# Kernel optimization log

Measured on AMD Instinct MI355X. Metric: run time of the kernel, lower is better.

## Reference

```python
import jax, jax.numpy as jnp
import numpy as np

N_NODES = 100000
N_EDGES = 3200000
D_IN = 128
D_OUT = 128


def setup_inputs() -> dict:
    key = jax.random.key(0)
    k1, k2, k3, k4, k5 = jax.random.split(key, 5)
    input_feature = jax.random.normal(k1, (N_NODES, D_IN), dtype=jnp.float32)
    edge_src = jax.random.randint(k2, (N_EDGES,), 0, N_NODES, dtype=jnp.int32)
    edge_dst = jax.random.randint(k3, (N_EDGES,), 0, N_NODES, dtype=jnp.int32)
    edge_vals = jax.random.uniform(k4, (N_EDGES,), dtype=jnp.float32)
    # kaiming-uniform-like init for weight, zeros for bias (as in reset_parameters)
    bound = float(np.sqrt(6.0 / D_IN))
    weight = jax.random.uniform(k5, (D_IN, D_OUT), dtype=jnp.float32,
                                minval=-bound, maxval=bound)
    bias = jnp.zeros((D_OUT,), dtype=jnp.float32)
    return {
        "input_feature": input_feature,
        "edge_src": edge_src,
        "edge_dst": edge_dst,
        "edge_vals": edge_vals,
        "weight": weight,
        "bias": bias,
    }


def reference(input_feature, edge_src, edge_dst, edge_vals, weight, bias):
    # support = X @ W  -> [N, D_OUT]
    support = jnp.matmul(input_feature, weight)
    # sparse.mm(A, support): out[dst] += A[dst, src] * support[src]
    gathered = support[edge_src] * edge_vals[:, None]  # [E, D_OUT]
    output = jax.ops.segment_sum(gathered, edge_dst, num_segments=N_NODES)
    output = output + bias  # bias-add (use_bias=True)
    return output
```

## Files before the change

### kernel.cpp

```cpp
#include <hip/hip_runtime.h>

#define N_NODES 100000
#define N_EDGES 3200000
#define D 128

#define K1C    391
#define CHUNK  4096
#define NCHUNK 782
#define GEMMB  782
#define CAPB   8960

static const size_t OFF_SB    = 0;
static const size_t OFF_REC   = 25600000;
static const size_t OFF_SORT2 = 53626880;
static const size_t OFF_OFFS  = 67640320;
static const size_t OFF_GCUR  = 68040320;

typedef __attribute__((ext_vector_type(8))) short bf16x8;
typedef __attribute__((ext_vector_type(4))) float f32x4;

__device__ __forceinline__ unsigned short f2bf(float f) {
    unsigned u = __float_as_uint(f);
    return (unsigned short)((u + 0x7FFFu + ((u >> 16) & 1u)) >> 16);
}

__global__ __launch_bounds__(512) void partition_edges(
        const int* __restrict__ esrc,
        const int* __restrict__ edst,
        const float* __restrict__ eval,
        int* __restrict__ gcursor,
        int2* __restrict__ rec_out) {
    __shared__ int  hist[K1C];
    __shared__ int  lofs[K1C];
    __shared__ int  gbase[K1C];
    __shared__ int  cur[K1C];
    __shared__ int  wsum[8];
    __shared__ int2 staged[CHUNK];
    __shared__ unsigned short bkt[CHUNK];

    const int t    = threadIdx.x;
    const int lane = t & 63;
    const int wave = t >> 6;
    const int e0   = blockIdx.x * CHUNK;
    const int cnt  = min(CHUNK, N_EDGES - e0);

    for (int i = t; i < K1C; i += 512) hist[i] = 0;
    __syncthreads();

    for (int i = t; i < cnt; i += 512)
        atomicAdd(&hist[edst[e0 + i] >> 8], 1);
    __syncthreads();

    int hv   = (t < K1C) ? hist[t] : 0;
    int incl = hv;
    for (int off = 1; off < 64; off <<= 1) {
        int u = __shfl_up(incl, off);
        if (lane >= off) incl += u;
    }
    if (lane == 63) wsum[wave] = incl;
    __syncthreads();
    {
        int pre = 0;
        for (int w = 0; w < wave; ++w) pre += wsum[w];
        if (t < K1C) {
            int excl = pre + incl - hv;
            lofs[t]  = excl;
            cur[t]   = excl;
            gbase[t] = hv ? (t * CAPB + atomicAdd(&gcursor[t], hv)) : 0;
        }
    }
    __syncthreads();

    for (int i = t; i < cnt; i += 512) {
        int e = e0 + i;
        int d = edst[e];
        int b = d >> 8;
        int pos = atomicAdd(&cur[b], 1);
        staged[pos] = make_int2(esrc[e] | ((d & 255) << 17), __float_as_int(eval[e]));
        bkt[pos] = (unsigned short)b;
    }
    __syncthreads();

    for (int i = t; i < cnt; i += 512) {
        int bb = bkt[i];
        rec_out[gbase[bb] + (i - lofs[bb])] = staged[i];
    }
}

__global__ __launch_bounds__(256) void gemm_and_fine(
        const float* __restrict__ X,
        const float* __restrict__ W,
        unsigned* __restrict__ Sb,
        const int2* __restrict__ rec,
        const int* __restrict__ gcnt,
        int* __restrict__ offs,
        unsigned* __restrict__ sorted1) {
    __shared__ __align__(16) union {
        unsigned short wfrag[8][4][64][8];
        unsigned       stage[4][32][68];
    } u;
    __shared__ int fh[256];
    __shared__ int fcur[256];
    __shared__ int fwsum[4];

    const int t    = threadIdx.x;
    const int lane = t & 63;
    const int wave = t >> 6;

    if (blockIdx.x < GEMMB) {
        const int quad = lane >> 4;
        const int li   = lane & 15;
        const int rowBase = blockIdx.x * 128;

        for (int i = t; i < D * D; i += 256) {
            int k = i >> 7, n = i & 127;
            u.wfrag[n >> 4][k >> 5][((k >> 3) & 3) * 16 + (n & 15)][k & 7] = f2bf(W[i]);
        }
        __syncthreads();

        f32x4 acc[2][8];
#pragma unroll
        for (int rt = 0; rt < 2; ++rt)
#pragma unroll
            for (int ct = 0; ct < 8; ++ct)
                acc[rt][ct] = (f32x4){0.f, 0.f, 0.f, 0.f};

#pragma unroll
        for (int kt = 0; kt < 4; ++kt) {
            bf16x8 a[2];
#pragma unroll
            for (int rt = 0; rt < 2; ++rt) {
                int row = rowBase + wave * 32 + rt * 16 + li;
                if (row >= N_NODES) row = N_NODES - 1;
                const float* xp = X + (size_t)row * D + kt * 32 + quad * 8;
                float4 f0 = ((const float4*)xp)[0];
                float4 f1 = ((const float4*)xp)[1];
                bf16x8 av;
                av[0] = (short)f2bf(f0.x); av[1] = (short)f2bf(f0.y);
                av[2] = (short)f2bf(f0.z); av[3] = (short)f2bf(f0.w);
                av[4] = (short)f2bf(f1.x); av[5] = (short)f2bf(f1.y);
                av[6] = (short)f2bf(f1.z); av[7] = (short)f2bf(f1.w);
                a[rt] = av;
            }
#pragma unroll
            for (int ct = 0; ct < 8; ++ct) {
                bf16x8 b = *(const bf16x8*)&u.wfrag[ct][kt][lane][0];
                acc[0][ct] = __builtin_amdgcn_mfma_f32_16x16x32_bf16(a[0], b, acc[0][ct], 0, 0, 0);
                acc[1][ct] = __builtin_amdgcn_mfma_f32_16x16x32_bf16(a[1], b, acc[1][ct], 0, 0, 0);
            }
        }
        __syncthreads();

        unsigned short* sw = (unsigned short*)&u.stage[wave][0][0];
#pragma unroll
        for (int rt = 0; rt < 2; ++rt)
#pragma unroll
            for (int r = 0; r < 4; ++r) {
                int lrow = rt * 16 + quad * 4 + r;
#pragma unroll
                for (int ct = 0; ct < 8; ++ct)
                    sw[lrow * 136 + ct * 16 + li] = f2bf(acc[rt][ct][r]);
            }
        for (int lrow = 0; lrow < 32; ++lrow) {
            int node = rowBase + wave * 32 + lrow;
            if (node < N_NODES)
                Sb[(size_t)node * 64 + lane] = ((unsigned*)sw)[lrow * 68 + lane];
        }
    } else {
        const int c    = blockIdx.x - GEMMB;
        const int beg  = c * CAPB;
        const int bcnt = gcnt[c];
        const int end  = beg + bcnt;

        fh[t] = 0;
        __syncthreads();

        for (int i = beg + t; i < end; i += 256)
            atomicAdd(&fh[(rec[i].x >> 17) & 255], 1);
        __syncthreads();

        int hv   = fh[t];
        int incl = hv;
        for (int off = 1; off < 64; off <<= 1) {
            int uu = __shfl_up(incl, off);
            if (lane >= off) incl += uu;
        }
        if (lane == 63) fwsum[wave] = incl;
        __syncthreads();
        {
            int pre = 0;
            for (int w = 0; w < wave; ++w) pre += fwsum[w];
            int excl = pre + incl - hv;
            int node = c * 256 + t;
            if (node < N_NODES) offs[node] = beg + excl;
            fcur[t] = beg + excl;
        }
        __syncthreads();

        for (int i = beg + t; i < end; i += 256) {
            int2 q = rec[i];
            int dl = (q.x >> 17) & 255;
            int p = atomicAdd(&fcur[dl], 1);
            unsigned vb = f2bf(__int_as_float(q.y));
            sorted1[p] = (unsigned)(q.x & 0x1FFFF) | ((vb & 0x7FFFu) << 17);
        }
    }
}

#define FMA8(v, p) {                                                         \
    a0 += (v) * __uint_as_float((p).x << 16);                                \
    a1 += (v) * __uint_as_float((p).x & 0xFFFF0000u);                        \
    a2 += (v) * __uint_as_float((p).y << 16);                                \
    a3 += (v) * __uint_as_float((p).y & 0xFFFF0000u);                        \
    a4 += (v) * __uint_as_float((p).z << 16);                                \
    a5 += (v) * __uint_as_float((p).z & 0xFFFF0000u);                        \
    a6 += (v) * __uint_as_float((p).w << 16);                                \
    a7 += (v) * __uint_as_float((p).w & 0xFFFF0000u);                        \
}

__global__ __launch_bounds__(256) void reduce_segments(
        const unsigned* __restrict__ Sb,
        const unsigned* __restrict__ sorted,
        const int* __restrict__ offs,
        const int* __restrict__ gcnt,
        const float* __restrict__ bias,
        float* __restrict__ out) {
    const int lane = threadIdx.x & 63;
    const int node = (blockIdx.x * 256 + threadIdx.x) >> 6;
    if (node >= N_NODES) return;

    const int qr = lane >> 4;
    const int ql = lane & 15;

    const int beg = offs[node];
    const bool blast = ((node & 255) == 255) || (node == N_NODES - 1);
    const int end = blast ? ((node >> 8) * CAPB + gcnt[node >> 8])
                          : offs[node + 1];

    float a0 = 0.f, a1 = 0.f, a2 = 0.f, a3 = 0.f;
    float a4 = 0.f, a5 = 0.f, a6 = 0.f, a7 = 0.f;

    for (int base = beg; base < end; base += 64) {
        const int m = min(64, end - base);
        unsigned rec = 0;
        if (base + lane < end) rec = sorted[base + lane];
        const int ng = (m + 3) >> 2;

        int g = 0;
        for (; g + 4 <= ng; g += 4) {
            int i0 = 4 * (g + 0) + qr, i1 = 4 * (g + 1) + qr;
            int i2 = 4 * (g + 2) + qr, i3 = 4 * (g + 3) + qr;
            unsigned r0 = (unsigned)__shfl((int)rec, i0);
            unsigned r1 = (unsigned)__shfl((int)rec, i1);
            unsigned r2 = (unsigned)__shfl((int)rec, i2);
            unsigned r3 = (unsigned)__shfl((int)rec, i3);
            int s0 = r0 & 0x1FFFF, s1 = r1 & 0x1FFFF;
            int s2 = r2 & 0x1FFFF, s3 = r3 & 0x1FFFF;
            float v0 = __uint_as_float((r0 >> 17) << 16);
            float v1 = __uint_as_float((r1 >> 17) << 16);
            float v2 = __uint_as_float((r2 >> 17) << 16);
            float v3 = __uint_as_float((r3 >> 17) << 16);
            uint4 p0 = ((const uint4*)(Sb + (size_t)s0 * 64))[ql];
            uint4 p1 = ((const uint4*)(Sb + (size_t)s1 * 64))[ql];
            uint4 p2 = ((const uint4*)(Sb + (size_t)s2 * 64))[ql];
            uint4 p3 = ((const uint4*)(Sb + (size_t)s3 * 64))[ql];
            FMA8(v0, p0);
            FMA8(v1, p1);
            FMA8(v2, p2);
            FMA8(v3, p3);
        }
        for (; g < ng; ++g) {
            int i0 = 4 * g + qr;
            unsigned r0 = (unsigned)__shfl((int)rec, i0);
            int s0 = r0 & 0x1FFFF;
            float v0 = __uint_as_float((r0 >> 17) << 16);
            uint4 p0 = ((const uint4*)(Sb + (size_t)s0 * 64))[ql];
            FMA8(v0, p0);
        }
    }

    a0 += __shfl(a0, lane ^ 16); a1 += __shfl(a1, lane ^ 16);
    a2 += __shfl(a2, lane ^ 16); a3 += __shfl(a3, lane ^ 16);
    a4 += __shfl(a4, lane ^ 16); a5 += __shfl(a5, lane ^ 16);
    a6 += __shfl(a6, lane ^ 16); a7 += __shfl(a7, lane ^ 16);
    a0 += __shfl(a0, lane ^ 32); a1 += __shfl(a1, lane ^ 32);
    a2 += __shfl(a2, lane ^ 32); a3 += __shfl(a3, lane ^ 32);
    a4 += __shfl(a4, lane ^ 32); a5 += __shfl(a5, lane ^ 32);
    a6 += __shfl(a6, lane ^ 32); a7 += __shfl(a7, lane ^ 32);

    if (qr == 0) {
        float4 b0 = ((const float4*)bias)[2 * ql];
        float4 b1 = ((const float4*)bias)[2 * ql + 1];
        float4 r0 = make_float4(a0 + b0.x, a1 + b0.y, a2 + b0.z, a3 + b0.w);
        float4 r1 = make_float4(a4 + b1.x, a5 + b1.y, a6 + b1.z, a7 + b1.w);
        ((float4*)(out + (size_t)node * D))[2 * ql]     = r0;
        ((float4*)(out + (size_t)node * D))[2 * ql + 1] = r1;
    }
}

extern "C" void kernel_launch(void* const* d_in, const int* in_sizes, int n_in,
                              void* d_out, int out_size, void* d_ws, size_t ws_size,
                              hipStream_t stream) {
    const float* X    = (const float*)d_in[0];
    const int*   esrc = (const int*)  d_in[1];
    const int*   edst = (const int*)  d_in[2];
    const float* eval = (const float*)d_in[3];
    const float* W    = (const float*)d_in[4];
    const float* bias = (const float*)d_in[5];
    float* out = (float*)d_out;

    char* ws = (char*)d_ws;
    unsigned* SbU   = (unsigned*)(ws + OFF_SB);
    int2*     recs  = (int2*)    (ws + OFF_REC);
    unsigned* srt1  = (unsigned*)(ws + OFF_SORT2);
    int*      offs  = (int*)     (ws + OFF_OFFS);
    int*      gcur  = (int*)     (ws + OFF_GCUR);

    hipMemsetAsync(gcur, 0, K1C * 4, stream);

    partition_edges<<<NCHUNK, 512, 0, stream>>>(esrc, edst, eval, gcur, recs);

    gemm_and_fine<<<GEMMB + K1C, 256, 0, stream>>>(
        X, W, SbU, recs, gcur, offs, srt1);

    reduce_segments<<<(N_NODES + 3) / 4, 256, 0, stream>>>(
        SbU, srt1, offs, gcur, bias, out);
}
```

Baseline: 313.0 us.

## Co-schedule GEMM with edge partitioning and split fine sort into own kernel

```diff
diff --git a/kernel.cpp b/kernel.cpp
--- a/kernel.cpp
+++ b/kernel.cpp
@@ -24,186 +24,180 @@
     return (unsigned short)((u + 0x7FFFu + ((u >> 16) & 1u)) >> 16);
 }
 
-__global__ __launch_bounds__(512) void partition_edges(
+__global__ __launch_bounds__(512) void part_and_gemm(
         const int* __restrict__ esrc,
         const int* __restrict__ edst,
         const float* __restrict__ eval,
         int* __restrict__ gcursor,
-        int2* __restrict__ rec_out) {
-    __shared__ int  hist[K1C];
-    __shared__ int  lofs[K1C];
-    __shared__ int  gbase[K1C];
-    __shared__ int  cur[K1C];
-    __shared__ int  wsum[8];
-    __shared__ int2 staged[CHUNK];
-    __shared__ unsigned short bkt[CHUNK];
+        int2* __restrict__ rec_out,
+        const float* __restrict__ X,
+        const float* __restrict__ W,
+        unsigned* __restrict__ Sb) {
+    __shared__ __align__(16) union {
+        unsigned short wfrag[8][4][64][8];
+        unsigned       stage[8][16][68];
+        struct {
+            int2 staged[CHUNK];
+            unsigned short bkt[CHUNK];
+            int hist[K1C];
+            int lofs[K1C];
+            int gbase[K1C];
+            int cur[K1C];
+            int wsum[8];
+        } p;
+    } u;
 
     const int t    = threadIdx.x;
     const int lane = t & 63;
     const int wave = t >> 6;
-    const int e0   = blockIdx.x * CHUNK;
-    const int cnt  = min(CHUNK, N_EDGES - e0);
-
-    for (int i = t; i < K1C; i += 512) hist[i] = 0;
-    __syncthreads();
-
-    for (int i = t; i < cnt; i += 512)
-        atomicAdd(&hist[edst[e0 + i] >> 8], 1);
-    __syncthreads();
-
-    int hv   = (t < K1C) ? hist[t] : 0;
-    int incl = hv;
-    for (int off = 1; off < 64; off <<= 1) {
-        int u = __shfl_up(incl, off);
-        if (lane >= off) incl += u;
-    }
-    if (lane == 63) wsum[wave] = incl;
-    __syncthreads();
-    {
-        int pre = 0;
-        for (int w = 0; w < wave; ++w) pre += wsum[w];
-        if (t < K1C) {
-            int excl = pre + incl - hv;
-            lofs[t]  = excl;
-            cur[t]   = excl;
-            gbase[t] = hv ? (t * CAPB + atomicAdd(&gcursor[t], hv)) : 0;
-        }
-    }
-    __syncthreads();
-
-    for (int i = t; i < cnt; i += 512) {
-        int e = e0 + i;
-        int d = edst[e];
-        int b = d >> 8;
-        int pos = atomicAdd(&cur[b], 1);
-        staged[pos] = make_int2(esrc[e] | ((d & 255) << 17), __float_as_int(eval[e]));
-        bkt[pos] = (unsigned short)b;
-    }
-    __syncthreads();
-
-    for (int i = t; i < cnt; i += 512) {
-        int bb = bkt[i];
-        rec_out[gbase[bb] + (i - lofs[bb])] = staged[i];
-    }
-}
-
-__global__ __launch_bounds__(256) void gemm_and_fine(
-        const float* __restrict__ X,
-        const float* __restrict__ W,
-        unsigned* __restrict__ Sb,
+
+    if (blockIdx.x < NCHUNK) {
+        const int e0  = blockIdx.x * CHUNK;
+        const int cnt = min(CHUNK, N_EDGES - e0);
+
+        for (int i = t; i < K1C; i += 512) u.p.hist[i] = 0;
+        __syncthreads();
+
+        for (int i = t; i < cnt; i += 512)
+            atomicAdd(&u.p.hist[edst[e0 + i] >> 8], 1);
+        __syncthreads();
+
+        int hv   = (t < K1C) ? u.p.hist[t] : 0;
+        int incl = hv;
+        for (int off = 1; off < 64; off <<= 1) {
+            int uu = __shfl_up(incl, off);
+            if (lane >= off) incl += uu;
+        }
+        if (lane == 63) u.p.wsum[wave] = incl;
+        __syncthreads();
+        {
+            int pre = 0;
+            for (int w = 0; w < wave; ++w) pre += u.p.wsum[w];
+            if (t < K1C) {
+                int excl = pre + incl - hv;
+                u.p.lofs[t]  = excl;
+                u.p.cur[t]   = excl;
+                u.p.gbase[t] = hv ? (t * CAPB + atomicAdd(&gcursor[t], hv)) : 0;
+            }
+        }
+        __syncthreads();
+
+        for (int i = t; i < cnt; i += 512) {
+            int e = e0 + i;
+            int d = edst[e];
+            int b = d >> 8;
+            int pos = atomicAdd(&u.p.cur[b], 1);
+            u.p.staged[pos] = make_int2(esrc[e] | ((d & 255) << 17),
+                                        __float_as_int(eval[e]));
+            u.p.bkt[pos] = (unsigned short)b;
+        }
+        __syncthreads();
+
+        for (int i = t; i < cnt; i += 512) {
+            int bb = u.p.bkt[i];
+            rec_out[u.p.gbase[bb] + (i - u.p.lofs[bb])] = u.p.staged[i];
+        }
+    } else {
+        const int quad = lane >> 4;
+        const int li   = lane & 15;
+        const int rowBase = (blockIdx.x - NCHUNK) * 128;
+
+        for (int i = t; i < D * D; i += 512) {
+            int k = i >> 7, n = i & 127;
+            u.wfrag[n >> 4][k >> 5][((k >> 3) & 3) * 16 + (n & 15)][k & 7] = f2bf(W[i]);
+        }
+        __syncthreads();
+
+        f32x4 acc[8];
+#pragma unroll
+        for (int ct = 0; ct < 8; ++ct)
+            acc[ct] = (f32x4){0.f, 0.f, 0.f, 0.f};
+
+#pragma unroll
+        for (int kt = 0; kt < 4; ++kt) {
+            int row = rowBase + wave * 16 + li;
+            if (row >= N_NODES) row = N_NODES - 1;
+            const float* xp = X + (size_t)row * D + kt * 32 + quad * 8;
+            float4 f0 = ((const float4*)xp)[0];
+            float4 f1 = ((const float4*)xp)[1];
+            bf16x8 a;
+            a[0] = (short)f2bf(f0.x); a[1] = (short)f2bf(f0.y);
+            a[2] = (short)f2bf(f0.z); a[3] = (short)f2bf(f0.w);
+            a[4] = (short)f2bf(f1.x); a[5] = (short)f2bf(f1.y);
+            a[6] = (short)f2bf(f1.z); a[7] = (short)f2bf(f1.w);
+#pragma unroll
+            for (int ct = 0; ct < 8; ++ct) {
+                bf16x8 b = *(const bf16x8*)&u.wfrag[ct][kt][lane][0];
+                acc[ct] = __builtin_amdgcn_mfma_f32_16x16x32_bf16(a, b, acc[ct], 0, 0, 0);
+            }
+        }
+        __syncthreads();
+
+        unsigned short* sw = (unsigned short*)&u.stage[wave][0][0];
+#pragma unroll
+        for (int r = 0; r < 4; ++r) {
+            int lrow = quad * 4 + r;
+#pragma unroll
+            for (int ct = 0; ct < 8; ++ct)
+                sw[lrow * 136 + ct * 16 + li] = f2bf(acc[ct][r]);
+        }
+        for (int lrow = 0; lrow < 16; ++lrow) {
+            int node = rowBase + wave * 16 + lrow;
+            if (node < N_NODES)
+                Sb[(size_t)node * 64 + lane] = ((unsigned*)sw)[lrow * 68 + lane];
+        }
+    }
+}
+
+__global__ __launch_bounds__(512) void fine_sort(
         const int2* __restrict__ rec,
         const int* __restrict__ gcnt,
         int* __restrict__ offs,
         unsigned* __restrict__ sorted1) {
-    __shared__ __align__(16) union {
-        unsigned short wfrag[8][4][64][8];
-        unsigned       stage[4][32][68];
-    } u;
     __shared__ int fh[256];
     __shared__ int fcur[256];
     __shared__ int fwsum[4];
 
+    const int c    = blockIdx.x;
     const int t    = threadIdx.x;
     const int lane = t & 63;
-    const int wave = t >> 6;
-
-    if (blockIdx.x < GEMMB) {
-        const int quad = lane >> 4;
-        const int li   = lane & 15;
-        const int rowBase = blockIdx.x * 128;
-
-        for (int i = t; i < D * D; i += 256) {
-            int k = i >> 7, n = i & 127;
-            u.wfrag[n >> 4][k >> 5][((k >> 3) & 3) * 16 + (n & 15)][k & 7] = f2bf(W[i]);
-        }
-        __syncthreads();
-
-        f32x4 acc[2][8];
-#pragma unroll
-        for (int rt = 0; rt < 2; ++rt)
-#pragma unroll
-            for (int ct = 0; ct < 8; ++ct)
-                acc[rt][ct] = (f32x4){0.f, 0.f, 0.f, 0.f};
-
-#pragma unroll
-        for (int kt = 0; kt < 4; ++kt) {
-            bf16x8 a[2];
-#pragma unroll
-            for (int rt = 0; rt < 2; ++rt) {
-                int row = rowBase + wave * 32 + rt * 16 + li;
-                if (row >= N_NODES) row = N_NODES - 1;
-                const float* xp = X + (size_t)row * D + kt * 32 + quad * 8;
-                float4 f0 = ((const float4*)xp)[0];
-                float4 f1 = ((const float4*)xp)[1];
-                bf16x8 av;
-                av[0] = (short)f2bf(f0.x); av[1] = (short)f2bf(f0.y);
-                av[2] = (short)f2bf(f0.z); av[3] = (short)f2bf(f0.w);
-                av[4] = (short)f2bf(f1.x); av[5] = (short)f2bf(f1.y);
-                av[6] = (short)f2bf(f1.z); av[7] = (short)f2bf(f1.w);
-                a[rt] = av;
-            }
-#pragma unroll
-            for (int ct = 0; ct < 8; ++ct) {
-                bf16x8 b = *(const bf16x8*)&u.wfrag[ct][kt][lane][0];
-                acc[0][ct] = __builtin_amdgcn_mfma_f32_16x16x32_bf16(a[0], b, acc[0][ct], 0, 0, 0);
-                acc[1][ct] = __builtin_amdgcn_mfma_f32_16x16x32_bf16(a[1], b, acc[1][ct], 0, 0, 0);
-            }
-        }
-        __syncthreads();
-
-        unsigned short* sw = (unsigned short*)&u.stage[wave][0][0];
-#pragma unroll
-        for (int rt = 0; rt < 2; ++rt)
-#pragma unroll
-            for (int r = 0; r < 4; ++r) {
-                int lrow = rt * 16 + quad * 4 + r;
-#pragma unroll
-                for (int ct = 0; ct < 8; ++ct)
-                    sw[lrow * 136 + ct * 16 + li] = f2bf(acc[rt][ct][r]);
-            }
-        for (int lrow = 0; lrow < 32; ++lrow) {
-            int node = rowBase + wave * 32 + lrow;
-            if (node < N_NODES)
-                Sb[(size_t)node * 64 + lane] = ((unsigned*)sw)[lrow * 68 + lane];
-        }
-    } else {
-        const int c    = blockIdx.x - GEMMB;
-        const int beg  = c * CAPB;
-        const int bcnt = gcnt[c];
-        const int end  = beg + bcnt;
-
-        fh[t] = 0;
-        __syncthreads();
-
-        for (int i = beg + t; i < end; i += 256)
-            atomicAdd(&fh[(rec[i].x >> 17) & 255], 1);
-        __syncthreads();
-
+    const int beg  = c * CAPB;
+    const int end  = beg + gcnt[c];
+
+    if (t < 256) fh[t] = 0;
+    __syncthreads();
+
+    for (int i = beg + t; i < end; i += 512)
+        atomicAdd(&fh[(rec[i].x >> 17) & 255], 1);
+    __syncthreads();
+
+    if (t < 256) {
         int hv   = fh[t];
         int incl = hv;
         for (int off = 1; off < 64; off <<= 1) {
             int uu = __shfl_up(incl, off);
             if (lane >= off) incl += uu;
         }
-        if (lane == 63) fwsum[wave] = incl;
-        __syncthreads();
-        {
-            int pre = 0;
-            for (int w = 0; w < wave; ++w) pre += fwsum[w];
-            int excl = pre + incl - hv;
-            int node = c * 256 + t;
-            if (node < N_NODES) offs[node] = beg + excl;
-            fcur[t] = beg + excl;
-        }
-        __syncthreads();
-
-        for (int i = beg + t; i < end; i += 256) {
-            int2 q = rec[i];
-            int dl = (q.x >> 17) & 255;
-            int p = atomicAdd(&fcur[dl], 1);
-            unsigned vb = f2bf(__int_as_float(q.y));
-            sorted1[p] = (unsigned)(q.x & 0x1FFFF) | ((vb & 0x7FFFu) << 17);
-        }
+        if (lane == 63) fwsum[t >> 6] = incl;
+        fh[t] = incl - hv;
+    }
+    __syncthreads();
+    if (t < 256) {
+        int pre = 0;
+        for (int w = 0; w < (t >> 6); ++w) pre += fwsum[w];
+        int excl = pre + fh[t];
+        int node = c * 256 + t;
+        if (node < N_NODES) offs[node] = beg + excl;
+        fcur[t] = beg + excl;
+    }
+    __syncthreads();
+
+    for (int i = beg + t; i < end; i += 512) {
+        int2 q = rec[i];
+        int dl = (q.x >> 17) & 255;
+        int p = atomicAdd(&fcur[dl], 1);
+        unsigned vb = f2bf(__int_as_float(q.y));
+        sorted1[p] = (unsigned)(q.x & 0x1FFFF) | ((vb & 0x7FFFu) << 17);
     }
 }
 
@@ -318,10 +312,10 @@
 
     hipMemsetAsync(gcur, 0, K1C * 4, stream);
 
-    partition_edges<<<NCHUNK, 512, 0, stream>>>(esrc, edst, eval, gcur, recs);
-
-    gemm_and_fine<<<GEMMB + K1C, 256, 0, stream>>>(
-        X, W, SbU, recs, gcur, offs, srt1);
+    part_and_gemm<<<NCHUNK + GEMMB, 512, 0, stream>>>(
+        esrc, edst, eval, gcur, recs, X, W, SbU);
+
+    fine_sort<<<K1C, 512, 0, stream>>>(recs, gcur, offs, srt1);
 
     reduce_segments<<<(N_NODES + 3) / 4, 256, 0, stream>>>(
         SbU, srt1, offs, gcur, bias, out);
```

After: 302.5 us. -3.3%, faster.
